# Optimization experiments

Measured on AMD Instinct MI355X. Metric: run time of the kernel, lower is better.

Reference implementation:

```python
import jax, jax.numpy as jnp
import numpy as np

B, S, H, Z = 32, 2048, 256, 64
TEMPERATURE = float(H) ** 0.5
NEG_INF = -1e9


def setup_inputs() -> dict:
    key = jax.random.key(0)
    ks = jax.random.split(key, 8)
    return {
        "encoder_hidden_states": jax.random.normal(ks[0], (B, S, H), dtype=jnp.float32),
        "decoder_hidden_states": jax.random.normal(ks[1], (B, S, H), dtype=jnp.float32),
        "decoder_final_hidden_state": jax.random.normal(ks[2], (B, H), dtype=jnp.float32),
        "latent_z_seq": jax.random.normal(ks[3], (B, S, Z), dtype=jnp.float32),
        "mask": jax.random.randint(ks[4], (B, S), 0, 2).astype(bool),
        "Wq": jax.random.normal(ks[5], (H, H), dtype=jnp.float32),
        "Wk": jax.random.normal(ks[6], (H, H), dtype=jnp.float32),
        "Wv": jax.random.normal(ks[7], (Z, Z), dtype=jnp.float32),
    }


def reference(encoder_hidden_states, decoder_hidden_states, decoder_final_hidden_state,
              latent_z_seq, mask, Wq, Wk, Wv):
    # Projections
    k = jnp.einsum('bsh,hd->bsd', encoder_hidden_states, Wk)
    q = jnp.einsum('bsh,hd->bsd', decoder_hidden_states, Wq)
    v = jnp.einsum('bsz,zd->bsd', latent_z_seq, Wv)
    # alignment[b, i, j] = q_i . k_j / sqrt(H)   -> [B, S, S]
    alignment = jnp.einsum('bid,bjd->bij', q, k) / TEMPERATURE
    # mask over QUERY positions (axis -2), broadcast along key axis (-1)
    alignment = jnp.where(mask[:, :, None], alignment, NEG_INF)
    # NOTE: non-standard softmax over the query axis (dim=-2)
    attn = jax.nn.softmax(alignment, axis=-2)
    output = jnp.einsum('bij,bjd->bid', attn, v)  # [B, S, Z]
    return output, attn
```

## Files before the change

kernel.cpp:

```cpp
#include <hip/hip_runtime.h>
#include <stdint.h>

#define B_  32
#define S_  2048
#define H_  256
#define Z_  64

typedef unsigned short u16;
typedef __attribute__((ext_vector_type(8))) short bf16x8;
typedef __attribute__((ext_vector_type(4))) float f32x4;

__device__ __forceinline__ u16 f2bf(float f) {
    unsigned int x = __float_as_uint(f);
    x = (x + 0x7fffu + ((x >> 16) & 1u)) >> 16;
    return (u16)x;
}
__device__ __forceinline__ float bf2f(u16 u) {
    return __uint_as_float(((unsigned int)u) << 16);
}

__device__ __forceinline__ void gl2lds16(const void* g, void* l) {
    __builtin_amdgcn_global_load_lds(
        (const __attribute__((address_space(1))) unsigned int*)g,
        (__attribute__((address_space(3))) unsigned int*)l,
        16, 0, 0);
}

__global__ void detect_kernel(const u16* __restrict__ wq, int* __restrict__ flag) {
    __shared__ int tot;
    const int t = threadIdx.x;
    if (t == 0) tot = 0;
    __syncthreads();
    int cnt = 0;
    #pragma unroll
    for (int r = 0; r < 16; ++r) {
        u16 u = wq[(r * 256 + t) * 2];
        int e = (u >> 7) & 0xFF;
        cnt += (u == 0 || (e >= 107 && e <= 132)) ? 1 : 0;
    }
    atomicAdd(&tot, cnt);
    __syncthreads();
    if (t == 0) *flag = (tot < 2048) ? 1 : 0;
}

__device__ void role_mask(int bx, const void* __restrict__ raw, int* __restrict__ mi) {
    __shared__ int isByte;
    const int t = threadIdx.x;
    if (t == 0) isByte = 0;
    __syncthreads();
    const unsigned int* w = (const unsigned int*)raw;
    if (w[t & 255] > 1u) isByte = 1;
    __syncthreads();
    int e = bx * 256 + t;
    int val;
    if (isByte) val = ((const unsigned char*)raw)[e] ? 1 : 0;
    else        val = w[e] ? 1 : 0;
    mi[e] = val;
}

__device__ void role_wsplit(int bx, int by, int fp32,
                            const void* __restrict__ Wq, const void* __restrict__ Wk,
                            u16* __restrict__ WqTh, u16* __restrict__ WqTl,
                            u16* __restrict__ WkTh, u16* __restrict__ WkTl) {
    const void* src = by ? Wk : Wq;
    u16* oh = by ? WkTh : WqTh;
    u16* ol = by ? WkTl : WqTl;
    int base = bx * 1024;
    #pragma unroll
    for (int r = 0; r < 4; ++r) {
        int idx = base + r * 256 + threadIdx.x;
        int d = idx >> 8, h = idx & 255;
        float v = fp32 ? ((const float*)src)[h * 256 + d]
                       : bf2f(((const u16*)src)[h * 256 + d]);
        u16 hi = f2bf(v);
        oh[idx] = hi;
        ol[idx] = f2bf(v - bf2f(hi));
    }
}

__device__ void role_xsplit(int bx, int by, int fp32,
                            const void* __restrict__ dec, const void* __restrict__ enc,
                            u16* __restrict__ Xdh, u16* __restrict__ Xdl,
                            u16* __restrict__ Xeh, u16* __restrict__ Xel) {
    const void* src = by ? enc : dec;
    u16* oh = by ? Xeh : Xdh;
    u16* ol = by ? Xel : Xdl;
    const int t = threadIdx.x;
    const size_t blockbase = (size_t)bx * 4096;
    if (fp32) {
        const float4* s4 = (const float4*)src;
        #pragma unroll
        for (int j = 0; j < 4; ++j) {
            size_t idx = blockbase + j * 1024 + t * 4;
            float4 v = s4[idx >> 2];
            u16 h0 = f2bf(v.x), h1 = f2bf(v.y), h2 = f2bf(v.z), h3 = f2bf(v.w);
            u16 l0 = f2bf(v.x - bf2f(h0)), l1 = f2bf(v.y - bf2f(h1));
            u16 l2 = f2bf(v.z - bf2f(h2)), l3 = f2bf(v.w - bf2f(h3));
            uint2 ph, pl;
            ph.x = (unsigned)h0 | ((unsigned)h1 << 16);
            ph.y = (unsigned)h2 | ((unsigned)h3 << 16);
            pl.x = (unsigned)l0 | ((unsigned)l1 << 16);
            pl.y = (unsigned)l2 | ((unsigned)l3 << 16);
            ((uint2*)oh)[idx >> 2] = ph;
            ((uint2*)ol)[idx >> 2] = pl;
        }
    } else {
        const uint2* s2 = (const uint2*)src;
        #pragma unroll
        for (int j = 0; j < 4; ++j) {
            size_t idx = blockbase + j * 1024 + t * 4;
            uint2 r = s2[idx >> 2];
            uint2 z; z.x = 0u; z.y = 0u;
            ((uint2*)oh)[idx >> 2] = r;
            ((uint2*)ol)[idx >> 2] = z;
        }
    }
}

__device__ void role_vproj(int bx, int dc, int fp32,
                           const void* __restrict__ Lraw,
                           const void* __restrict__ Wvraw, u16* __restrict__ vT) {
    __shared__ float wv[64 * 16];
    const int t = threadIdx.x;
    #pragma unroll
    for (int r = 0; r < 4; ++r) {
        int idx = r * 256 + t;
        int z = idx >> 4, dd = idx & 15;
        wv[idx] = fp32 ? ((const float*)Wvraw)[z * 64 + dc * 16 + dd]
                       : bf2f(((const u16*)Wvraw)[z * 64 + dc * 16 + dd]);
    }
    __syncthreads();
    const int flat = bx * 256 + t;
    const int b = flat >> 11, s = flat & 2047;

    float lz[64];
    if (fp32) {
        const float4* lr = (const float4*)((const float*)Lraw + (size_t)flat * 64);
        #pragma unroll
        for (int c = 0; c < 16; ++c) {
            float4 v = lr[c];
            lz[c * 4 + 0] = v.x; lz[c * 4 + 1] = v.y;
            lz[c * 4 + 2] = v.z; lz[c * 4 + 3] = v.w;
        }
    } else {
        const uint4* lr = (const uint4*)((const u16*)Lraw + (size_t)flat * 64);
        #pragma unroll
        for (int c = 0; c < 8; ++c) {
            uint4 v = lr[c];
            unsigned wd[4] = {v.x, v.y, v.z, v.w};
            #pragma unroll
            for (int e2 = 0; e2 < 4; ++e2) {
                lz[c * 8 + e2 * 2 + 0] = bf2f((u16)(wd[e2] & 0xffffu));
                lz[c * 8 + e2 * 2 + 1] = bf2f((u16)(wd[e2] >> 16));
            }
        }
    }

    float acc[16];
    #pragma unroll
    for (int d = 0; d < 16; ++d) acc[d] = 0.f;
    for (int z = 0; z < 64; ++z) {
        float lv = lz[z];
        const float4* wrow = (const float4*)&wv[z * 16];
        #pragma unroll
        for (int d4 = 0; d4 < 4; ++d4) {
            float4 wq = wrow[d4];
            acc[d4 * 4 + 0] += lv * wq.x;
            acc[d4 * 4 + 1] += lv * wq.y;
            acc[d4 * 4 + 2] += lv * wq.z;
            acc[d4 * 4 + 3] += lv * wq.w;
        }
    }
    #pragma unroll
    for (int d = 0; d < 16; ++d)
        vT[((size_t)b * 64 + dc * 16 + d) * S_ + s] = f2bf(acc[d]);
}

__global__ __launch_bounds__(256) void prep_kernel(
        const int* __restrict__ flagp, int n_xs,
        const void* __restrict__ dec, const void* __restrict__ enc,
        u16* __restrict__ Xdh, u16* __restrict__ Xdl,
        u16* __restrict__ Xeh, u16* __restrict__ Xel,
        const void* __restrict__ Lraw, const void* __restrict__ Wvraw,
        u16* __restrict__ vT,
        const void* __restrict__ Wq, const void* __restrict__ Wk,
        u16* __restrict__ WqTh, u16* __restrict__ WqTl,
        u16* __restrict__ WkTh, u16* __restrict__ WkTl,
        const void* __restrict__ mraw, int* __restrict__ maskI)
{
    const int fp32 = *flagp;
    int r = blockIdx.x;
    if (r < n_xs) {
        role_xsplit(r & 4095, r >> 12, fp32, dec, enc, Xdh, Xdl, Xeh, Xel);
        return;
    }
    r -= n_xs;
    if (r < 1024) {
        role_vproj(r & 255, r >> 8, fp32, Lraw, Wvraw, vT);
        return;
    }
    r -= 1024;
    if (r < 128) {
        role_wsplit(r & 63, r >> 6, fp32, Wq, Wk, WqTh, WqTl, WkTh, WkTl);
        return;
    }
    r -= 128;
    role_mask(r, mraw, maskI);
}

__global__ __launch_bounds__(256, 2) void proj_kernel(
        const int* __restrict__ flagp, int use_xsplit,
        const float* __restrict__ Xf0, const u16* __restrict__ Xu0,
        const u16* __restrict__ Xh0, const u16* __restrict__ Xl0,
        const u16* __restrict__ WTh0, const u16* __restrict__ WTl0,
        u16* __restrict__ Ph0, u16* __restrict__ Pl0,
        const float* __restrict__ Xf1, const u16* __restrict__ Xu1,
        const u16* __restrict__ Xh1, const u16* __restrict__ Xl1,
        const u16* __restrict__ WTh1, const u16* __restrict__ WTl1,
        u16* __restrict__ Ph1, u16* __restrict__ Pl1)
{
    __shared__ __align__(16) u16 lds[16384];
    const int z = blockIdx.z;
    const float* Xf = z ? Xf1 : Xf0;
    const u16*   Xu = z ? Xu1 : Xu0;
    const u16*   Xh = z ? Xh1 : Xh0;
    const u16*   Xl = z ? Xl1 : Xl0;
    const u16*  WTh = z ? WTh1 : WTh0;
    const u16*  WTl = z ? WTl1 : WTl0;
    u16* Ph = z ? Ph1 : Ph0;
    u16* Pl = z ? Pl1 : Pl0;

    const int fp32 = *flagp;
    const int t = threadIdx.x;
    const int lane = t & 63, w = t >> 6;
    const int i0 = blockIdx.x * 128;
    const int d0 = blockIdx.y * 128;
    const int rh = w >> 1, ch = w & 1;
    const int l15 = lane & 15;
    const int c0 = lane >> 4;

    const int srow = t >> 3;
    const int scp  = t & 7;
    const int sc   = scp ^ (srow & 7);
    const int scol = (sc & 3) * 8;
    const int slo  = sc & 4;

    f32x4 acc[4][4];
    #pragma unroll
    for (int a = 0; a < 4; ++a)
        #pragma unroll
        for (int c = 0; c < 4; ++c) acc[a][c] = (f32x4){0.f, 0.f, 0.f, 0.f};

    for (int ks = 0; ks < 8; ++ks) {
        const int kc = ks * 32;
        {
            const u16* wsrc = slo ? WTl : WTh;
            #pragma unroll
            for (int rep = 0; rep < 4; ++rep) {
                int s = t + rep * 256;
                int row = srow + rep * 32;
                gl2lds16(wsrc + (size_t)(d0 + row) * H_ + kc + scol, lds + 8192 + s * 8);
            }
        }
        if (use_xsplit) {
            const u16* xsrc = slo ? Xl : Xh;
            #pragma unroll
            for (int rep = 0; rep < 4; ++rep) {
                int s = t + rep * 256;
                int row = srow + rep * 32;
                gl2lds16(xsrc + (size_t)(i0 + row) * H_ + kc + scol, lds + s * 8);
            }
        } else if (fp32) {
            #pragma unroll
            for (int rep = 0; rep < 2; ++rep) {
                int s = t + rep * 256;
                int r = s >> 2, c8 = s & 3;
                const float4* src = (const float4*)(Xf + (size_t)(i0 + r) * H_ + kc + c8 * 8);
                float4 x0 = src[0], x1 = src[1];
                float xs[8] = {x0.x, x0.y, x0.z, x0.w, x1.x, x1.y, x1.z, x1.w};
                unsigned hh[8], ll[8];
                #pragma unroll
                for (int j = 0; j < 8; ++j) {
                    u16 hb = f2bf(xs[j]);
                    hh[j] = hb;
                    ll[j] = f2bf(xs[j] - bf2f(hb));
                }
                uint4 ph, pl;
                ph.x = hh[0] | (hh[1] << 16); ph.y = hh[2] | (hh[3] << 16);
                ph.z = hh[4] | (hh[5] << 16); ph.w = hh[6] | (hh[7] << 16);
                pl.x = ll[0] | (ll[1] << 16); pl.y = ll[2] | (ll[3] << 16);
                pl.z = ll[4] | (ll[5] << 16); pl.w = ll[6] | (ll[7] << 16);
                int posH = c8 ^ (r & 7);
                *(uint4*)(lds + r * 64 + posH * 8) = ph;
                *(uint4*)(lds + r * 64 + (posH ^ 4) * 8) = pl;
            }
        } else {
            #pragma unroll
            for (int rep = 0; rep < 2; ++rep) {
                int s = t + rep * 256;
                int r = s >> 2, c8 = s & 3;
                uint4 raw = *(const uint4*)(Xu + (size_t)(i0 + r) * H_ + kc + c8 * 8);
                int posH = c8 ^ (r & 7);
                *(uint4*)(lds + r * 64 + posH * 8) = raw;
                *(uint4*)(lds + r * 64 + (posH ^ 4) * 8) = (uint4){0u, 0u, 0u, 0u};
            }
        }
        __syncthreads();
        bf16x8 ah[4], al[4], bh[4], bl[4];
        #pragma unroll
        for (int f = 0; f < 4; ++f) {
            int ra = rh * 64 + f * 16 + l15;
            int rb = ch * 64 + f * 16 + l15;
            int pa = c0 ^ (ra & 7);
            int pb = c0 ^ (rb & 7);
            ah[f] = *(const bf16x8*)(lds + ra * 64 + pa * 8);
            al[f] = *(const bf16x8*)(lds + ra * 64 + (pa ^ 4) * 8);
            bh[f] = *(const bf16x8*)(lds + 8192 + rb * 64 + pb * 8);
            bl[f] = *(const bf16x8*)(lds + 8192 + rb * 64 + (pb ^ 4) * 8);
        }
        #pragma unroll
        for (int fr = 0; fr < 4; ++fr)
            #pragma unroll
            for (int fc = 0; fc < 4; ++fc) {
                acc[fr][fc] = __builtin_amdgcn_mfma_f32_16x16x32_bf16(al[fr], bh[fc], acc[fr][fc], 0, 0, 0);
                acc[fr][fc] = __builtin_amdgcn_mfma_f32_16x16x32_bf16(ah[fr], bl[fc], acc[fr][fc], 0, 0, 0);
                acc[fr][fc] = __builtin_amdgcn_mfma_f32_16x16x32_bf16(ah[fr], bh[fc], acc[fr][fc], 0, 0, 0);
            }
        __syncthreads();
    }
    #pragma unroll
    for (int fr = 0; fr < 4; ++fr)
        #pragma unroll
        for (int fc = 0; fc < 4; ++fc)
            #pragma unroll
            for (int reg = 0; reg < 4; ++reg) {
                float v = acc[fr][fc][reg];
                int i = i0 + rh * 64 + fr * 16 + (lane >> 4) * 4 + reg;
                int d = d0 + ch * 64 + fc * 16 + l15;
                u16 hi = f2bf(v);
                u16 lo = f2bf(v - bf2f(hi));
                size_t off = (size_t)i * H_ + d;
                Ph[off] = hi;
                Pl[off] = lo;
            }
}

__global__ __launch_bounds__(256, 2) void qk_kernel(
        const u16* __restrict__ qh, const u16* __restrict__ ql,
        const u16* __restrict__ kh, const u16* __restrict__ kl,
        const int* __restrict__ maskI, u16* __restrict__ attnB,
        float* __restrict__ attnF, u16* __restrict__ stageB, int use_stage,
        float* __restrict__ m_p, float* __restrict__ s_p,
        int b0, const int* __restrict__ flagp)
{
    __shared__ __align__(16) char smem[35328];
    u16*  stage = (u16*)smem;
    u16*  etile = (u16*)smem;
    float* cmax = (float*)(smem + 32768);
    float* csum = (float*)(smem + 33792);
    float* mrow = (float*)(smem + 34816);

    const int fp32 = *flagp;
    const int t = threadIdx.x;
    const int lane = t & 63, w = t >> 6;
    const int jt = blockIdx.x, it = blockIdx.y, bz = blockIdx.z;
    const int b = b0 + bz;
    const int i0 = it * 128, j0 = jt * 128;
    const int rh = w >> 1, ch = w & 1;
    const int l15 = lane & 15;
    const int c0 = lane >> 4;

    if (t < 128) mrow[t] = (maskI[b * S_ + i0 + t] != 0) ? 1.f : 0.f;

    const size_t qbase = ((size_t)bz * S_ + i0) * H_;
    const size_t kbase = ((size_t)bz * S_ + j0) * H_;

    const int srow = t >> 3;
    const int scp  = t & 7;
    const int sc   = scp ^ (srow & 7);
    const int scol = (sc & 3) * 8;
    const u16* qsrc = (sc & 4) ? ql : qh;
    const u16* ksrc = (sc & 4) ? kl : kh;

    f32x4 acc[4][4];
    #pragma unroll
    for (int a = 0; a < 4; ++a)
        #pragma unroll
        for (int c = 0; c < 4; ++c) acc[a][c] = (f32x4){0.f, 0.f, 0.f, 0.f};

    for (int ks = 0; ks < 8; ++ks) {
        const int kc = ks * 32;
        #pragma unroll
        for (int rep = 0; rep < 4; ++rep) {
            int s = t + rep * 256;
            int row = srow + rep * 32;
            gl2lds16(qsrc + qbase + (size_t)row * H_ + kc + scol, stage + s * 8);
            gl2lds16(ksrc + kbase + (size_t)row * H_ + kc + scol, stage + 8192 + s * 8);
        }
        __syncthreads();
        bf16x8 ah[4], al[4], bh[4], bl[4];
        #pragma unroll
        for (int f = 0; f < 4; ++f) {
            int ra = rh * 64 + f * 16 + l15;
            int rb = ch * 64 + f * 16 + l15;
            int pa = c0 ^ (ra & 7);
            int pb = c0 ^ (rb & 7);
            ah[f] = *(const bf16x8*)(stage + ra * 64 + pa * 8);
            al[f] = *(const bf16x8*)(stage + ra * 64 + (pa ^ 4) * 8);
            bh[f] = *(const bf16x8*)(stage + 8192 + rb * 64 + pb * 8);
            bl[f] = *(const bf16x8*)(stage + 8192 + rb * 64 + (pb ^ 4) * 8);
        }
        #pragma unroll
        for (int fr = 0; fr < 4; ++fr)
            #pragma unroll
            for (int fc = 0; fc < 4; ++fc) {
                acc[fr][fc] = __builtin_amdgcn_mfma_f32_16x16x32_bf16(al[fr], bh[fc], acc[fr][fc], 0, 0, 0);
                acc[fr][fc] = __builtin_amdgcn_mfma_f32_16x16x32_bf16(ah[fr], bl[fc], acc[fr][fc], 0, 0, 0);
                acc[fr][fc] = __builtin_amdgcn_mfma_f32_16x16x32_bf16(ah[fr], bh[fc], acc[fr][fc], 0, 0, 0);
            }
        __syncthreads();
    }

    const float inv_t = 0.0625f;
    float mloc[4] = {-3e38f, -3e38f, -3e38f, -3e38f};
    #pragma unroll
    for (int fr = 0; fr < 4; ++fr)
        #pragma unroll
        for (int reg = 0; reg < 4; ++reg) {
            float keep = mrow[rh * 64 + fr * 16 + (lane >> 4) * 4 + reg];
            #pragma unroll
            for (int fc = 0; fc < 4; ++fc) {
                float l = acc[fr][fc][reg] * inv_t;
                l = (keep != 0.f) ? l : -1e9f;
                acc[fr][fc][reg] = l;
                mloc[fc] = fmaxf(mloc[fc], l);
            }
        }
    #pragma unroll
    for (int fc = 0; fc < 4; ++fc) {
        mloc[fc] = fmaxf(mloc[fc], __shfl_xor(mloc[fc], 16, 64));
        mloc[fc] = fmaxf(mloc[fc], __shfl_xor(mloc[fc], 32, 64));
    }
    if (lane < 16) {
        #pragma unroll
        for (int fc = 0; fc < 4; ++fc)
            cmax[rh * 128 + ch * 64 + fc * 16 + lane] = mloc[fc];
    }
    __syncthreads();

    float mcol[4], sloc[4];
    #pragma unroll
    for (int fc = 0; fc < 4; ++fc) {
        int c = ch * 64 + fc * 16 + l15;
        mcol[fc] = fmaxf(cmax[c], cmax[128 + c]);
        sloc[fc] = 0.f;
    }
    #pragma unroll
    for (int fr = 0; fr < 4; ++fr)
        #pragma unroll
        for (int reg = 0; reg < 4; ++reg) {
            int row = rh * 64 + fr * 16 + (lane >> 4) * 4 + reg;
            #pragma unroll
            for (int fc = 0; fc < 4; ++fc) {
                float e = __expf(acc[fr][fc][reg] - mcol[fc]);
                sloc[fc] += e;
                etile[row * 128 + ch * 64 + fc * 16 + l15] = f2bf(e);
            }
        }
    #pragma unroll
    for (int fc = 0; fc < 4; ++fc) {
        sloc[fc] += __shfl_xor(sloc[fc], 16, 64);
        sloc[fc] += __shfl_xor(sloc[fc], 32, 64);
    }
    if (lane < 16) {
        #pragma unroll
        for (int fc = 0; fc < 4; ++fc)
            csum[rh * 128 + ch * 64 + fc * 16 + lane] = sloc[fc];
    }
    __syncthreads();

    if (t < 128) {
        float m = fmaxf(cmax[t], cmax[128 + t]);
        float sres = csum[t] + csum[128 + t];
        size_t so = ((size_t)b * 16 + it) * S_ + j0 + t;
        m_p[so] = m;
        s_p[so] = sres;
    }
    const size_t abase = ((size_t)b * S_ + i0) * S_ + j0;
    if (fp32) {
        if (use_stage) {
            #pragma unroll
            for (int rep = 0; rep < 8; ++rep) {
                int s = t + rep * 256;
                int row = s >> 4, off = (s & 15) * 8;
                *(uint4*)(stageB + abase + (size_t)row * S_ + off) = *(const uint4*)(etile + s * 8);
            }
        } else {
            #pragma unroll
            for (int rep = 0; rep < 8; ++rep) {
                int s = t + rep * 256;
                int row = s >> 4, off = (s & 15) * 8;
                const u16* src = etile + s * 8;
                float* gp = attnF + abase + (size_t)row * S_ + off;
                float4 f0, f1;
                f0.x = bf2f(src[0]); f0.y = bf2f(src[1]); f0.z = bf2f(src[2]); f0.w = bf2f(src[3]);
                f1.x = bf2f(src[4]); f1.y = bf2f(src[5]); f1.z = bf2f(src[6]); f1.w = bf2f(src[7]);
                *(float4*)gp = f0;
                *(float4*)(gp + 4) = f1;
            }
        }
    } else {
        #pragma unroll
        for (int rep = 0; rep < 8; ++rep) {
            int s = t + rep * 256;
            int row = s >> 4, off = (s & 15) * 8;
            *(uint4*)(attnB + abase + (size_t)row * S_ + off) = *(const uint4*)(etile + s * 8);
        }
    }
}

__global__ __launch_bounds__(256) void stats_kernel(
        const float* __restrict__ m_p, const float* __restrict__ s_p, float* __restrict__ scl)
{
    int id = blockIdx.x * 256 + threadIdx.x;
    int b = id >> 11, j = id & 2047;
    float mv[16];
    float M = -3e38f;
    #pragma unroll
    for (int itile = 0; itile < 16; ++itile) {
        mv[itile] = m_p[((size_t)b * 16 + itile) * S_ + j];
        M = fmaxf(M, mv[itile]);
    }
    float L = 0.f;
    #pragma unroll
    for (int itile = 0; itile < 16; ++itile)
        L += s_p[((size_t)b * 16 + itile) * S_ + j] * __expf(mv[itile] - M);
    float invL = (L > 0.f) ? (1.f / L) : 0.f;
    #pragma unroll
    for (int itile = 0; itile < 16; ++itile)
        scl[((size_t)b * 16 + itile) * S_ + j] = __expf(mv[itile] - M) * invL;
}

__global__ __launch_bounds__(256, 2) void av_gemm_kernel(
        const u16* __restrict__ vT, const float* __restrict__ scl,
        const u16* __restrict__ stageB, u16* __restrict__ attnB,
        float* __restrict__ attnF,
        u16* __restrict__ outB, float* __restrict__ outF,
        const int* __restrict__ flagp)
{
    __shared__ __align__(16) u16 lds_attn[128 * 128];
    __shared__ __align__(16) u16 lds_vt[64 * 128];
    const int fp32 = *flagp;
    const u16* srcE = fp32 ? stageB : attnB;
    const int t = threadIdx.x;
    const int lane = t & 63, w = t >> 6;
    const int it = blockIdx.x, b = blockIdx.y;
    const int i0 = it * 128;
    const int l15 = lane & 15;

    const int acp = t & 15;
    const int arow0 = t >> 4;
    const int ac = acp ^ (arow0 & 15);
    const int vpos = (t & 15) ^ (t >> 4);
    const int j8 = (t & 15) * 8;

    f32x4 acc[2][4];
    #pragma unroll
    for (int a = 0; a < 2; ++a)
        #pragma unroll
        for (int c = 0; c < 4; ++c) acc[a][c] = (f32x4){0.f, 0.f, 0.f, 0.f};

    for (int jt = 0; jt < 16; ++jt) {
        const int j0 = jt * 128;
        __syncthreads();
        const size_t abase = ((size_t)b * S_ + i0) * S_ + j0;
        #pragma unroll
        for (int rep = 0; rep < 8; ++rep) {
            int s = t + rep * 256;
            int row = arow0 + rep * 16;
            gl2lds16(srcE + abase + (size_t)row * S_ + ac * 8, lds_attn + s * 8);
        }
        float sc[8], esc[8];
        {
            const float4* sp = (const float4*)(scl + ((size_t)b * 16 + it) * S_ + j0 + j8);
            float4 s0 = sp[0], s1 = sp[1];
            sc[0] = s0.x; sc[1] = s0.y; sc[2] = s0.z; sc[3] = s0.w;
            sc[4] = s1.x; sc[5] = s1.y; sc[6] = s1.z; sc[7] = s1.w;
            const float4* ep = (const float4*)(scl + ((size_t)b * 16 + it) * S_ + j0 + ac * 8);
            float4 e0 = ep[0], e1 = ep[1];
            esc[0] = e0.x; esc[1] = e0.y; esc[2] = e0.z; esc[3] = e0.w;
            esc[4] = e1.x; esc[5] = e1.y; esc[6] = e1.z; esc[7] = e1.w;
        }
        #pragma unroll
        for (int rep = 0; rep < 4; ++rep) {
            int d = (t >> 4) + rep * 16;
            uint4 raw = *(const uint4*)(vT + ((size_t)b * 64 + d) * S_ + j0 + j8);
            unsigned wd[4] = {raw.x, raw.y, raw.z, raw.w};
            #pragma unroll
            for (int e2 = 0; e2 < 4; ++e2) {
                float f0 = bf2f((u16)(wd[e2] & 0xffffu)) * sc[e2 * 2];
                float f1 = bf2f((u16)(wd[e2] >> 16))     * sc[e2 * 2 + 1];
                wd[e2] = (unsigned)f2bf(f0) | ((unsigned)f2bf(f1) << 16);
            }
            uint4 pk; pk.x = wd[0]; pk.y = wd[1]; pk.z = wd[2]; pk.w = wd[3];
            *(uint4*)(lds_vt + d * 128 + vpos * 8) = pk;
        }
        __syncthreads();

        #pragma unroll
        for (int rep = 0; rep < 8; ++rep) {
            int s = t + rep * 256;
            int row = arow0 + rep * 16;
            uint4 pk = *(const uint4*)(lds_attn + s * 8);
            unsigned wd[4] = {pk.x, pk.y, pk.z, pk.w};
            float f[8];
            f[0] = bf2f((u16)(wd[0] & 0xffffu)) * esc[0];
            f[1] = bf2f((u16)(wd[0] >> 16))     * esc[1];
            f[2] = bf2f((u16)(wd[1] & 0xffffu)) * esc[2];
            f[3] = bf2f((u16)(wd[1] >> 16))     * esc[3];
            f[4] = bf2f((u16)(wd[2] & 0xffffu)) * esc[4];
            f[5] = bf2f((u16)(wd[2] >> 16))     * esc[5];
            f[6] = bf2f((u16)(wd[3] & 0xffffu)) * esc[6];
            f[7] = bf2f((u16)(wd[3] >> 16))     * esc[7];
            size_t ga = abase + (size_t)row * S_ + ac * 8;
            if (fp32) {
                float4 o0, o1;
                o0.x = f[0]; o0.y = f[1]; o0.z = f[2]; o0.w = f[3];
                o1.x = f[4]; o1.y = f[5]; o1.z = f[6]; o1.w = f[7];
                *(float4*)(attnF + ga) = o0;
                *(float4*)(attnF + ga + 4) = o1;
            } else {
                uint4 o;
                o.x = (unsigned)f2bf(f[0]) | ((unsigned)f2bf(f[1]) << 16);
                o.y = (unsigned)f2bf(f[2]) | ((unsigned)f2bf(f[3]) << 16);
                o.z = (unsigned)f2bf(f[4]) | ((unsigned)f2bf(f[5]) << 16);
                o.w = (unsigned)f2bf(f[6]) | ((unsigned)f2bf(f[7]) << 16);
                *(uint4*)(attnB + ga) = o;
            }
        }

        #pragma unroll
        for (int ksj = 0; ksj < 4; ++ksj) {
            int ck = ksj * 4 + (lane >> 4);
            int pA = ck ^ l15;
            int rA0 = w * 32 + l15, rA1 = w * 32 + 16 + l15;
            bf16x8 a0 = *(const bf16x8*)(lds_attn + rA0 * 128 + pA * 8);
            bf16x8 a1 = *(const bf16x8*)(lds_attn + rA1 * 128 + pA * 8);
            bf16x8 bb[4];
            #pragma unroll
            for (int fc = 0; fc < 4; ++fc) {
                int d = fc * 16 + l15;
                bb[fc] = *(const bf16x8*)(lds_vt + d * 128 + pA * 8);
            }
            #pragma unroll
            for (int fc = 0; fc < 4; ++fc) {
                acc[0][fc] = __builtin_amdgcn_mfma_f32_16x16x32_bf16(a0, bb[fc], acc[0][fc], 0, 0, 0);
                acc[1][fc] = __builtin_amdgcn_mfma_f32_16x16x32_bf16(a1, bb[fc], acc[1][fc], 0, 0, 0);
            }
        }
    }
    #pragma unroll
    for (int fr = 0; fr < 2; ++fr)
        #pragma unroll
        for (int fc = 0; fc < 4; ++fc)
            #pragma unroll
            for (int reg = 0; reg < 4; ++reg) {
                int i = i0 + w * 32 + fr * 16 + (lane >> 4) * 4 + reg;
                int d = fc * 16 + l15;
                float v = acc[fr][fc][reg];
                size_t oo = ((size_t)b * S_ + i) * Z_ + d;
                if (fp32) outF[oo] = v;
                else      outB[oo] = f2bf(v);
            }
}

__global__ __launch_bounds__(256, 2) void av_fallback_kernel(
        const u16* __restrict__ vT, const float* __restrict__ scl,
        u16* __restrict__ attnB, float* __restrict__ attnF,
        u16* __restrict__ outB, float* __restrict__ outF,
        const int* __restrict__ flagp)
{
    __shared__ __align__(16) u16 lds_attn[128 * 128];
    __shared__ __align__(16) u16 lds_vt[64 * 128];
    __shared__ float lds_scale[128];
    const int fp32 = *flagp;
    const int t = threadIdx.x;
    const int lane = t & 63, w = t >> 6;
    const int it = blockIdx.x, b = blockIdx.y;
    const int i0 = it * 128;
    const int l15 = lane & 15, koff = (lane >> 4) * 8;

    f32x4 acc[2][4];
    #pragma unroll
    for (int a = 0; a < 2; ++a)
        #pragma unroll
        for (int c = 0; c < 4; ++c) acc[a][c] = (f32x4){0.f, 0.f, 0.f, 0.f};

    for (int jt = 0; jt < 16; ++jt) {
        const int j0 = jt * 128;
        __syncthreads();
        if (t < 128) lds_scale[t] = scl[((size_t)b * 16 + it) * S_ + j0 + t];
        #pragma unroll
        for (int rep = 0; rep < 4; ++rep) {
            int s = t + rep * 256;
            int d = s >> 4, off = (s & 15) * 8;
            gl2lds16(vT + ((size_t)b * 64 + d) * S_ + j0 + off, lds_vt + s * 8);
        }
        __syncthreads();

        const size_t abase = ((size_t)b * S_ + i0) * S_ + j0;
        if (fp32) {
            #pragma unroll
            for (int rep = 0; rep < 8; ++rep) {
                int s = t + rep * 256;
                int row = s >> 4, off = (s & 15) * 8;
                float* gp = attnF + abase + (size_t)row * S_ + off;
                float4 p0 = *(const float4*)gp;
                float4 p1 = *(const float4*)(gp + 4);
                p0.x *= lds_scale[off + 0]; p0.y *= lds_scale[off + 1];
                p0.z *= lds_scale[off + 2]; p0.w *= lds_scale[off + 3];
                p1.x *= lds_scale[off + 4]; p1.y *= lds_scale[off + 5];
                p1.z *= lds_scale[off + 6]; p1.w *= lds_scale[off + 7];
                *(float4*)gp = p0;
                *(float4*)(gp + 4) = p1;
                uint4 pk;
                pk.x = (unsigned)f2bf(p0.x) | ((unsigned)f2bf(p0.y) << 16);
                pk.y = (unsigned)f2bf(p0.z) | ((unsigned)f2bf(p0.w) << 16);
                pk.z = (unsigned)f2bf(p1.x) | ((unsigned)f2bf(p1.y) << 16);
                pk.w = (unsigned)f2bf(p1.z) | ((unsigned)f2bf(p1.w) << 16);
                *(uint4*)(lds_attn + s * 8) = pk;
            }
        } else {
            #pragma unroll
            for (int rep = 0; rep < 8; ++rep) {
                int s = t + rep * 256;
                int row = s >> 4, off = (s & 15) * 8;
                size_t ga = abase + (size_t)row * S_ + off;
                uint4 pk = *(const uint4*)(attnB + ga);
                unsigned int wd[4] = {pk.x, pk.y, pk.z, pk.w};
                #pragma unroll
                for (int e2 = 0; e2 < 4; ++e2) {
                    float f0 = bf2f((u16)(wd[e2] & 0xffffu)) * lds_scale[off + e2 * 2];
                    float f1 = bf2f((u16)(wd[e2] >> 16))     * lds_scale[off + e2 * 2 + 1];
                    wd[e2] = (unsigned int)f2bf(f0) | ((unsigned int)f2bf(f1) << 16);
                }
                uint4 opk; opk.x = wd[0]; opk.y = wd[1]; opk.z = wd[2]; opk.w = wd[3];
                *(uint4*)(attnB + ga) = opk;
                *(uint4*)(lds_attn + s * 8) = opk;
            }
        }
        __syncthreads();

        #pragma unroll
        for (int ksj = 0; ksj < 4; ++ksj) {
            bf16x8 a0 = *(const bf16x8*)(lds_attn + (w * 32 +  0 + l15) * 128 + ksj * 32 + koff);
            bf16x8 a1 = *(const bf16x8*)(lds_attn + (w * 32 + 16 + l15) * 128 + ksj * 32 + koff);
            bf16x8 bb[4];
            #pragma unroll
            for (int fc = 0; fc < 4; ++fc)
                bb[fc] = *(const bf16x8*)(lds_vt + (fc * 16 + l15) * 128 + ksj * 32 + koff);
            #pragma unroll
            for (int fc = 0; fc < 4; ++fc) {
                acc[0][fc] = __builtin_amdgcn_mfma_f32_16x16x32_bf16(a0, bb[fc], acc[0][fc], 0, 0, 0);
                acc[1][fc] = __builtin_amdgcn_mfma_f32_16x16x32_bf16(a1, bb[fc], acc[1][fc], 0, 0, 0);
            }
        }
    }
    #pragma unroll
    for (int fr = 0; fr < 2; ++fr)
        #pragma unroll
        for (int fc = 0; fc < 4; ++fc)
            #pragma unroll
            for (int reg = 0; reg < 4; ++reg) {
                int i = i0 + w * 32 + fr * 16 + (lane >> 4) * 4 + reg;
                int d = fc * 16 + l15;
                float v = acc[fr][fc][reg];
                size_t oo = ((size_t)b * S_ + i) * Z_ + d;
                if (fp32) outF[oo] = v;
                else      outB[oo] = f2bf(v);
            }
}

extern "C" void kernel_launch(void* const* d_in, const int* in_sizes, int n_in,
                              void* d_out, int out_size, void* d_ws, size_t ws_size,
                              hipStream_t stream) {
    const void* enc    = d_in[0];
    const void* dec    = d_in[1];
    const void* latent = d_in[3];
    const void* mraw   = d_in[4];
    const void* Wq     = d_in[5];
    const void* Wk     = d_in[6];
    const void* Wv     = d_in[7];

    u16*   outB  = (u16*)d_out;
    float* outF  = (float*)d_out;
    u16*   attnB = outB + (size_t)B_ * S_ * Z_;
    float* attnF = outF + (size_t)B_ * S_ * Z_;
    float* m_p = (float*)d_out;
    float* s_p = m_p + (size_t)B_ * 16 * S_;

    char* ws = (char*)d_ws;
    int*   flag  = (int*)ws;
    int*   maskI = (int*)(ws + 256);
    u16*   vT    = (u16*)((char*)maskI + (size_t)B_ * S_ * 4);
    u16*   WqTh  = vT + (size_t)B_ * Z_ * S_;
    u16*   WqTl  = WqTh + H_ * H_;
    u16*   WkTh  = WqTl + H_ * H_;
    u16*   WkTl  = WkTh + H_ * H_;
    float* scl   = (float*)(WkTl + H_ * H_);
    char*  dyn   = (char*)(scl + (size_t)B_ * 16 * S_);

    const size_t fixed_bytes  = (size_t)(dyn - ws);
    const size_t per_batch    = (size_t)4 * S_ * H_ * 2;
    const size_t xsplit_bytes = (size_t)4 * B_ * S_ * H_ * 2;
    const size_t stage_bytes  = (size_t)B_ * S_ * S_ * 2;

    long long avail = (long long)ws_size - (long long)fixed_bytes;
    int use_xsplit = 0, use_stage = 0;
    u16 *Xdh = 0, *Xdl = 0, *Xeh = 0, *Xel = 0, *stageB = 0;
    if (avail >= (long long)(xsplit_bytes + per_batch)) {
        use_xsplit = 1;
        Xdh = (u16*)dyn;
        Xdl = Xdh + (size_t)B_ * S_ * H_;
        Xeh = Xdl + (size_t)B_ * S_ * H_;
        Xel = Xeh + (size_t)B_ * S_ * H_;
        dyn += xsplit_bytes;
        avail -= (long long)xsplit_bytes;
    }
    if (avail >= (long long)(stage_bytes + per_batch)) {
        use_stage = 1;
        stageB = (u16*)dyn;
        dyn += stage_bytes;
        avail -= (long long)stage_bytes;
    }
    int g_b = (avail > 0) ? (int)(avail / (long long)per_batch) : 1;
    if (g_b < 1)  g_b = 1;
    if (g_b > 32) g_b = 32;

    u16* qh = (u16*)dyn;
    u16* ql = qh + (size_t)g_b * S_ * H_;
    u16* kh = ql + (size_t)g_b * S_ * H_;
    u16* kl = kh + (size_t)g_b * S_ * H_;

    detect_kernel<<<dim3(1), 256, 0, stream>>>((const u16*)Wq, flag);

    const int n_xs = use_xsplit ? 8192 : 0;
    prep_kernel<<<dim3(n_xs + 1024 + 128 + 256), 256, 0, stream>>>(
        flag, n_xs, dec, enc, Xdh, Xdl, Xeh, Xel,
        latent, Wv, vT, Wq, Wk, WqTh, WqTl, WkTh, WkTl, mraw, maskI);

    for (int b0 = 0; b0 < B_; b0 += g_b) {
        int g = (B_ - b0 < g_b) ? (B_ - b0) : g_b;
        size_t eoff = (size_t)b0 * S_ * H_;
        proj_kernel<<<dim3(g * 16, 2, 2), 256, 0, stream>>>(
            flag, use_xsplit,
            (const float*)dec + eoff, (const u16*)dec + eoff,
            use_xsplit ? Xdh + eoff : (u16*)0, use_xsplit ? Xdl + eoff : (u16*)0,
            WqTh, WqTl, qh, ql,
            (const float*)enc + eoff, (const u16*)enc + eoff,
            use_xsplit ? Xeh + eoff : (u16*)0, use_xsplit ? Xel + eoff : (u16*)0,
            WkTh, WkTl, kh, kl);
        qk_kernel<<<dim3(16, 16, g), 256, 0, stream>>>(qh, ql, kh, kl, maskI,
                                                       attnB, attnF, stageB, use_stage,
                                                       m_p, s_p, b0, flag);
    }
    stats_kernel<<<dim3(256), 256, 0, stream>>>(m_p, s_p, scl);
    if (use_stage) {
        av_gemm_kernel<<<dim3(16, 32), 256, 0, stream>>>(vT, scl, stageB, attnB, attnF,
                                                         outB, outF, flag);
    } else {
        av_fallback_kernel<<<dim3(16, 32), 256, 0, stream>>>(vT, scl, attnB, attnF,
                                                             outB, outF, flag);
    }
}
```

Baseline: 1.106 ms.

## Fold Wq·Wk into G matrix and enlarge QK tiles to 256x256

```diff
diff --git a/kernel.cpp b/kernel.cpp
--- a/kernel.cpp
+++ b/kernel.cpp
@@ -78,6 +78,27 @@
     }
 }
 
+__device__ void role_gmat(int d, int fp32,
+                          const void* __restrict__ Wq, const void* __restrict__ Wk,
+                          u16* __restrict__ Gh, u16* __restrict__ Gl) {
+    __shared__ float wqrow[256];
+    const int t = threadIdx.x;
+    wqrow[t] = fp32 ? ((const float*)Wq)[d * 256 + t]
+                    : bf2f(((const u16*)Wq)[d * 256 + t]);
+    __syncthreads();
+    float s = 0.f;
+    if (fp32) {
+        const float* wk = (const float*)Wk + (size_t)t * 256;
+        for (int e = 0; e < 256; ++e) s += wqrow[e] * wk[e];
+    } else {
+        const u16* wk = (const u16*)Wk + (size_t)t * 256;
+        for (int e = 0; e < 256; ++e) s += wqrow[e] * bf2f(wk[e]);
+    }
+    u16 hi = f2bf(s);
+    Gh[d * 256 + t] = hi;
+    Gl[d * 256 + t] = f2bf(s - bf2f(hi));
+}
+
 __device__ void role_xsplit(int bx, int by, int fp32,
                             const void* __restrict__ dec, const void* __restrict__ enc,
                             u16* __restrict__ Xdh, u16* __restrict__ Xdl,
@@ -186,6 +207,7 @@
         const void* __restrict__ Wq, const void* __restrict__ Wk,
         u16* __restrict__ WqTh, u16* __restrict__ WqTl,
         u16* __restrict__ WkTh, u16* __restrict__ WkTl,
+        u16* __restrict__ Gh, u16* __restrict__ Gl,
         const void* __restrict__ mraw, int* __restrict__ maskI)
 {
     const int fp32 = *flagp;
@@ -205,7 +227,12 @@
         return;
     }
     r -= 128;
-    role_mask(r, mraw, maskI);
+    if (r < 256) {
+        role_mask(r, mraw, maskI);
+        return;
+    }
+    r -= 256;
+    role_gmat(r, fp32, Wq, Wk, Gh, Gl);
 }
 
 __global__ __launch_bounds__(256, 2) void proj_kernel(
@@ -345,7 +372,9 @@
             }
 }
 
-__global__ __launch_bounds__(256, 2) void qk_kernel(
+#define NIT_ 8
+#define EST_ 136
+__global__ __launch_bounds__(512, 2) void qk_kernel(
         const u16* __restrict__ qh, const u16* __restrict__ ql,
         const u16* __restrict__ kh, const u16* __restrict__ kl,
         const int* __restrict__ maskI, u16* __restrict__ attnB,
@@ -353,24 +382,24 @@
         float* __restrict__ m_p, float* __restrict__ s_p,
         int b0, const int* __restrict__ flagp)
 {
-    __shared__ __align__(16) char smem[35328];
+    __shared__ __align__(16) char smem[74752];
     u16*  stage = (u16*)smem;
     u16*  etile = (u16*)smem;
-    float* cmax = (float*)(smem + 32768);
-    float* csum = (float*)(smem + 33792);
-    float* mrow = (float*)(smem + 34816);
+    float* cmax = (float*)(smem + 69632);
+    float* csum = (float*)(smem + 71680);
+    float* mrow = (float*)(smem + 73728);
 
     const int fp32 = *flagp;
     const int t = threadIdx.x;
     const int lane = t & 63, w = t >> 6;
+    const int wr = w >> 2, wc = w & 3;
     const int jt = blockIdx.x, it = blockIdx.y, bz = blockIdx.z;
     const int b = b0 + bz;
-    const int i0 = it * 128, j0 = jt * 128;
-    const int rh = w >> 1, ch = w & 1;
+    const int i0 = it * 256, j0 = jt * 256;
     const int l15 = lane & 15;
     const int c0 = lane >> 4;
 
-    if (t < 128) mrow[t] = (maskI[b * S_ + i0 + t] != 0) ? 1.f : 0.f;
+    if (t < 256) mrow[t] = (maskI[b * S_ + i0 + t] != 0) ? 1.f : 0.f;
 
     const size_t qbase = ((size_t)bz * S_ + i0) * H_;
     const size_t kbase = ((size_t)bz * S_ + j0) * H_;
@@ -382,9 +411,9 @@
     const u16* qsrc = (sc & 4) ? ql : qh;
     const u16* ksrc = (sc & 4) ? kl : kh;
 
-    f32x4 acc[4][4];
-    #pragma unroll
-    for (int a = 0; a < 4; ++a)
+    f32x4 acc[8][4];
+    #pragma unroll
+    for (int a = 0; a < 8; ++a)
         #pragma unroll
         for (int c = 0; c < 4; ++c) acc[a][c] = (f32x4){0.f, 0.f, 0.f, 0.f};
 
@@ -392,42 +421,43 @@
         const int kc = ks * 32;
         #pragma unroll
         for (int rep = 0; rep < 4; ++rep) {
-            int s = t + rep * 256;
-            int row = srow + rep * 32;
+            int s = t + rep * 512;
+            int row = srow + rep * 64;
             gl2lds16(qsrc + qbase + (size_t)row * H_ + kc + scol, stage + s * 8);
-            gl2lds16(ksrc + kbase + (size_t)row * H_ + kc + scol, stage + 8192 + s * 8);
-        }
-        __syncthreads();
-        bf16x8 ah[4], al[4], bh[4], bl[4];
+            gl2lds16(ksrc + kbase + (size_t)row * H_ + kc + scol, stage + 16384 + s * 8);
+        }
+        __syncthreads();
+        bf16x8 bhf[4], blf[4];
         #pragma unroll
         for (int f = 0; f < 4; ++f) {
-            int ra = rh * 64 + f * 16 + l15;
-            int rb = ch * 64 + f * 16 + l15;
+            int rb = wc * 64 + f * 16 + l15;
+            int pb = c0 ^ (rb & 7);
+            bhf[f] = *(const bf16x8*)(stage + 16384 + rb * 64 + pb * 8);
+            blf[f] = *(const bf16x8*)(stage + 16384 + rb * 64 + (pb ^ 4) * 8);
+        }
+        #pragma unroll
+        for (int fr = 0; fr < 8; ++fr) {
+            int ra = wr * 128 + fr * 16 + l15;
             int pa = c0 ^ (ra & 7);
-            int pb = c0 ^ (rb & 7);
-            ah[f] = *(const bf16x8*)(stage + ra * 64 + pa * 8);
-            al[f] = *(const bf16x8*)(stage + ra * 64 + (pa ^ 4) * 8);
-            bh[f] = *(const bf16x8*)(stage + 8192 + rb * 64 + pb * 8);
-            bl[f] = *(const bf16x8*)(stage + 8192 + rb * 64 + (pb ^ 4) * 8);
-        }
-        #pragma unroll
-        for (int fr = 0; fr < 4; ++fr)
+            bf16x8 ahf = *(const bf16x8*)(stage + ra * 64 + pa * 8);
+            bf16x8 alf = *(const bf16x8*)(stage + ra * 64 + (pa ^ 4) * 8);
             #pragma unroll
             for (int fc = 0; fc < 4; ++fc) {
-                acc[fr][fc] = __builtin_amdgcn_mfma_f32_16x16x32_bf16(al[fr], bh[fc], acc[fr][fc], 0, 0, 0);
-                acc[fr][fc] = __builtin_amdgcn_mfma_f32_16x16x32_bf16(ah[fr], bl[fc], acc[fr][fc], 0, 0, 0);
-                acc[fr][fc] = __builtin_amdgcn_mfma_f32_16x16x32_bf16(ah[fr], bh[fc], acc[fr][fc], 0, 0, 0);
-            }
+                acc[fr][fc] = __builtin_amdgcn_mfma_f32_16x16x32_bf16(alf, bhf[fc], acc[fr][fc], 0, 0, 0);
+                acc[fr][fc] = __builtin_amdgcn_mfma_f32_16x16x32_bf16(ahf, blf[fc], acc[fr][fc], 0, 0, 0);
+                acc[fr][fc] = __builtin_amdgcn_mfma_f32_16x16x32_bf16(ahf, bhf[fc], acc[fr][fc], 0, 0, 0);
+            }
+        }
         __syncthreads();
     }
 
     const float inv_t = 0.0625f;
     float mloc[4] = {-3e38f, -3e38f, -3e38f, -3e38f};
     #pragma unroll
-    for (int fr = 0; fr < 4; ++fr)
+    for (int fr = 0; fr < 8; ++fr)
         #pragma unroll
         for (int reg = 0; reg < 4; ++reg) {
-            float keep = mrow[rh * 64 + fr * 16 + (lane >> 4) * 4 + reg];
+            float keep = mrow[wr * 128 + fr * 16 + c0 * 4 + reg];
             #pragma unroll
             for (int fc = 0; fc < 4; ++fc) {
                 float l = acc[fr][fc][reg] * inv_t;
@@ -444,29 +474,72 @@
     if (lane < 16) {
         #pragma unroll
         for (int fc = 0; fc < 4; ++fc)
-            cmax[rh * 128 + ch * 64 + fc * 16 + lane] = mloc[fc];
+            cmax[wr * 256 + wc * 64 + fc * 16 + lane] = mloc[fc];
     }
     __syncthreads();
 
-    float mcol[4], sloc[4];
+    float mcol[4];
     #pragma unroll
     for (int fc = 0; fc < 4; ++fc) {
-        int c = ch * 64 + fc * 16 + l15;
-        mcol[fc] = fmaxf(cmax[c], cmax[128 + c]);
-        sloc[fc] = 0.f;
-    }
-    #pragma unroll
-    for (int fr = 0; fr < 4; ++fr)
-        #pragma unroll
-        for (int reg = 0; reg < 4; ++reg) {
-            int row = rh * 64 + fr * 16 + (lane >> 4) * 4 + reg;
-            #pragma unroll
-            for (int fc = 0; fc < 4; ++fc) {
-                float e = __expf(acc[fr][fc][reg] - mcol[fc]);
-                sloc[fc] += e;
-                etile[row * 128 + ch * 64 + fc * 16 + l15] = f2bf(e);
-            }
-        }
+        int c = wc * 64 + fc * 16 + l15;
+        mcol[fc] = fmaxf(cmax[c], cmax[256 + c]);
+    }
+
+    float sloc[4] = {0.f, 0.f, 0.f, 0.f};
+    const int myp = wc >> 1;
+    const int lcb = (wc & 1) * 64;
+    for (int p = 0; p < 2; ++p) {
+        __syncthreads();
+        if (myp == p) {
+            #pragma unroll
+            for (int fr = 0; fr < 8; ++fr)
+                #pragma unroll
+                for (int reg = 0; reg < 4; ++reg) {
+                    int row = wr * 128 + fr * 16 + c0 * 4 + reg;
+                    #pragma unroll
+                    for (int fc = 0; fc < 4; ++fc) {
+                        float e = __expf(acc[fr][fc][reg] - mcol[fc]);
+                        sloc[fc] += e;
+                        etile[row * EST_ + lcb + fc * 16 + l15] = f2bf(e);
+                    }
+                }
+        }
+        __syncthreads();
+        const size_t abase = ((size_t)b * S_ + i0) * S_ + j0 + p * 128;
+        if (fp32) {
+            if (use_stage) {
+                #pragma unroll
+                for (int rep = 0; rep < 8; ++rep) {
+                    int g = t + rep * 512;
+                    int row = g >> 4, c4 = g & 15;
+                    *(uint4*)(stageB + abase + (size_t)row * S_ + c4 * 8) =
+                        *(const uint4*)(etile + row * EST_ + c4 * 8);
+                }
+            } else {
+                #pragma unroll
+                for (int rep = 0; rep < 8; ++rep) {
+                    int g = t + rep * 512;
+                    int row = g >> 4, c4 = g & 15;
+                    const u16* src = etile + row * EST_ + c4 * 8;
+                    float* gp = attnF + abase + (size_t)row * S_ + c4 * 8;
+                    float4 f0, f1;
+                    f0.x = bf2f(src[0]); f0.y = bf2f(src[1]); f0.z = bf2f(src[2]); f0.w = bf2f(src[3]);
+                    f1.x = bf2f(src[4]); f1.y = bf2f(src[5]); f1.z = bf2f(src[6]); f1.w = bf2f(src[7]);
+                    *(float4*)gp = f0;
+                    *(float4*)(gp + 4) = f1;
+                }
+            }
+        } else {
+            #pragma unroll
+            for (int rep = 0; rep < 8; ++rep) {
+                int g = t + rep * 512;
+                int row = g >> 4, c4 = g & 15;
+                *(uint4*)(attnB + abase + (size_t)row * S_ + c4 * 8) =
+                    *(const uint4*)(etile + row * EST_ + c4 * 8);
+            }
+        }
+    }
+
     #pragma unroll
     for (int fc = 0; fc < 4; ++fc) {
         sloc[fc] += __shfl_xor(sloc[fc], 16, 64);
@@ -475,47 +548,16 @@
     if (lane < 16) {
         #pragma unroll
         for (int fc = 0; fc < 4; ++fc)
-            csum[rh * 128 + ch * 64 + fc * 16 + lane] = sloc[fc];
+            csum[wr * 256 + wc * 64 + fc * 16 + lane] = sloc[fc];
     }
     __syncthreads();
 
-    if (t < 128) {
-        float m = fmaxf(cmax[t], cmax[128 + t]);
-        float sres = csum[t] + csum[128 + t];
-        size_t so = ((size_t)b * 16 + it) * S_ + j0 + t;
+    if (t < 256) {
+        float m = fmaxf(cmax[t], cmax[256 + t]);
+        float sres = csum[t] + csum[256 + t];
+        size_t so = ((size_t)b * NIT_ + it) * S_ + j0 + t;
         m_p[so] = m;
         s_p[so] = sres;
-    }
-    const size_t abase = ((size_t)b * S_ + i0) * S_ + j0;
-    if (fp32) {
-        if (use_stage) {
-            #pragma unroll
-            for (int rep = 0; rep < 8; ++rep) {
-                int s = t + rep * 256;
-                int row = s >> 4, off = (s & 15) * 8;
-                *(uint4*)(stageB + abase + (size_t)row * S_ + off) = *(const uint4*)(etile + s * 8);
-            }
-        } else {
-            #pragma unroll
-            for (int rep = 0; rep < 8; ++rep) {
-                int s = t + rep * 256;
-                int row = s >> 4, off = (s & 15) * 8;
-                const u16* src = etile + s * 8;
-                float* gp = attnF + abase + (size_t)row * S_ + off;
-                float4 f0, f1;
-                f0.x = bf2f(src[0]); f0.y = bf2f(src[1]); f0.z = bf2f(src[2]); f0.w = bf2f(src[3]);
-                f1.x = bf2f(src[4]); f1.y = bf2f(src[5]); f1.z = bf2f(src[6]); f1.w = bf2f(src[7]);
-                *(float4*)gp = f0;
-                *(float4*)(gp + 4) = f1;
-            }
-        }
-    } else {
-        #pragma unroll
-        for (int rep = 0; rep < 8; ++rep) {
-            int s = t + rep * 256;
-            int row = s >> 4, off = (s & 15) * 8;
-            *(uint4*)(attnB + abase + (size_t)row * S_ + off) = *(const uint4*)(etile + s * 8);
-        }
     }
 }
 
@@ -524,21 +566,21 @@
 {
     int id = blockIdx.x * 256 + threadIdx.x;
     int b = id >> 11, j = id & 2047;
-    float mv[16];
+    float mv[NIT_];
     float M = -3e38f;
     #pragma unroll
-    for (int itile = 0; itile < 16; ++itile) {
-        mv[itile] = m_p[((size_t)b * 16 + itile) * S_ + j];
+    for (int itile = 0; itile < NIT_; ++itile) {
+        mv[itile] = m_p[((size_t)b * NIT_ + itile) * S_ + j];
         M = fmaxf(M, mv[itile]);
     }
     float L = 0.f;
     #pragma unroll
-    for (int itile = 0; itile < 16; ++itile)
-        L += s_p[((size_t)b * 16 + itile) * S_ + j] * __expf(mv[itile] - M);
+    for (int itile = 0; itile < NIT_; ++itile)
+        L += s_p[((size_t)b * NIT_ + itile) * S_ + j] * __expf(mv[itile] - M);
     float invL = (L > 0.f) ? (1.f / L) : 0.f;
     #pragma unroll
-    for (int itile = 0; itile < 16; ++itile)
-        scl[((size_t)b * 16 + itile) * S_ + j] = __expf(mv[itile] - M) * invL;
+    for (int itile = 0; itile < NIT_; ++itile)
+        scl[((size_t)b * NIT_ + itile) * S_ + j] = __expf(mv[itile] - M) * invL;
 }
 
 __global__ __launch_bounds__(256, 2) void av_gemm_kernel(
@@ -563,6 +605,7 @@
     const int ac = acp ^ (arow0 & 15);
     const int vpos = (t & 15) ^ (t >> 4);
     const int j8 = (t & 15) * 8;
+    const size_t sclbase = ((size_t)b * NIT_ + (it >> 1)) * S_;
 
     f32x4 acc[2][4];
     #pragma unroll
@@ -582,11 +625,11 @@
         }
         float sc[8], esc[8];
         {
-            const float4* sp = (const float4*)(scl + ((size_t)b * 16 + it) * S_ + j0 + j8);
+            const float4* sp = (const float4*)(scl + sclbase + j0 + j8);
             float4 s0 = sp[0], s1 = sp[1];
             sc[0] = s0.x; sc[1] = s0.y; sc[2] = s0.z; sc[3] = s0.w;
             sc[4] = s1.x; sc[5] = s1.y; sc[6] = s1.z; sc[7] = s1.w;
-            const float4* ep = (const float4*)(scl + ((size_t)b * 16 + it) * S_ + j0 + ac * 8);
+            const float4* ep = (const float4*)(scl + sclbase + j0 + ac * 8);
             float4 e0 = ep[0], e1 = ep[1];
             esc[0] = e0.x; esc[1] = e0.y; esc[2] = e0.z; esc[3] = e0.w;
             esc[4] = e1.x; esc[5] = e1.y; esc[6] = e1.z; esc[7] = e1.w;
@@ -689,6 +732,7 @@
     const int it = blockIdx.x, b = blockIdx.y;
     const int i0 = it * 128;
     const int l15 = lane & 15, koff = (lane >> 4) * 8;
+    const size_t sclbase = ((size_t)b * NIT_ + (it >> 1)) * S_;
 
     f32x4 acc[2][4];
     #pragma unroll
@@ -699,7 +743,7 @@
     for (int jt = 0; jt < 16; ++jt) {
         const int j0 = jt * 128;
         __syncthreads();
-        if (t < 128) lds_scale[t] = scl[((size_t)b * 16 + it) * S_ + j0 + t];
+        if (t < 128) lds_scale[t] = scl[sclbase + j0 + t];
         #pragma unroll
         for (int rep = 0; rep < 4; ++rep) {
             int s = t + rep * 256;
@@ -797,7 +841,7 @@
     u16*   attnB = outB + (size_t)B_ * S_ * Z_;
     float* attnF = outF + (size_t)B_ * S_ * Z_;
     float* m_p = (float*)d_out;
-    float* s_p = m_p + (size_t)B_ * 16 * S_;
+    float* s_p = m_p + (size_t)B_ * NIT_ * S_;
 
     char* ws = (char*)d_ws;
     int*   flag  = (int*)ws;
@@ -807,8 +851,10 @@
     u16*   WqTl  = WqTh + H_ * H_;
     u16*   WkTh  = WqTl + H_ * H_;
     u16*   WkTl  = WkTh + H_ * H_;
-    float* scl   = (float*)(WkTl + H_ * H_);
-    char*  dyn   = (char*)(scl + (size_t)B_ * 16 * S_);
+    u16*   Gh    = WkTl + H_ * H_;
+    u16*   Gl    = Gh + H_ * H_;
+    float* scl   = (float*)(Gl + H_ * H_);
+    char*  dyn   = (char*)(scl + (size_t)B_ * NIT_ * S_);
 
     const size_t fixed_bytes  = (size_t)(dyn - ws);
     const size_t per_batch    = (size_t)4 * S_ * H_ * 2;
@@ -845,24 +891,36 @@
     detect_kernel<<<dim3(1), 256, 0, stream>>>((const u16*)Wq, flag);
 
     const int n_xs = use_xsplit ? 8192 : 0;
-    prep_kernel<<<dim3(n_xs + 1024 + 128 + 256), 256, 0, stream>>>(
+    prep_kernel<<<dim3(n_xs + 1024 + 128 + 256 + 256), 256, 0, stream>>>(
         flag, n_xs, dec, enc, Xdh, Xdl, Xeh, Xel,
-        latent, Wv, vT, Wq, Wk, WqTh, WqTl, WkTh, WkTl, mraw, maskI);
+        latent, Wv, vT, Wq, Wk, WqTh, WqTl, WkTh, WkTl, Gh, Gl, mraw, maskI);
 
     for (int b0 = 0; b0 < B_; b0 += g_b) {
         int g = (B_ - b0 < g_b) ? (B_ - b0) : g_b;
         size_t eoff = (size_t)b0 * S_ * H_;
-        proj_kernel<<<dim3(g * 16, 2, 2), 256, 0, stream>>>(
-            flag, use_xsplit,
-            (const float*)dec + eoff, (const u16*)dec + eoff,
-            use_xsplit ? Xdh + eoff : (u16*)0, use_xsplit ? Xdl + eoff : (u16*)0,
-            WqTh, WqTl, qh, ql,
-            (const float*)enc + eoff, (const u16*)enc + eoff,
-            use_xsplit ? Xeh + eoff : (u16*)0, use_xsplit ? Xel + eoff : (u16*)0,
-            WkTh, WkTl, kh, kl);
-        qk_kernel<<<dim3(16, 16, g), 256, 0, stream>>>(qh, ql, kh, kl, maskI,
-                                                       attnB, attnF, stageB, use_stage,
-                                                       m_p, s_p, b0, flag);
+        if (use_xsplit) {
+            proj_kernel<<<dim3(g * 16, 2, 1), 256, 0, stream>>>(
+                flag, use_xsplit,
+                (const float*)enc + eoff, (const u16*)enc + eoff,
+                Xeh + eoff, Xel + eoff,
+                Gh, Gl, kh, kl,
+                (const float*)enc + eoff, (const u16*)enc + eoff,
+                Xeh + eoff, Xel + eoff,
+                Gh, Gl, kh, kl);
+            qk_kernel<<<dim3(NIT_, NIT_, g), 512, 0, stream>>>(
+                Xdh + eoff, Xdl + eoff, kh, kl, maskI,
+                attnB, attnF, stageB, use_stage, m_p, s_p, b0, flag);
+        } else {
+            proj_kernel<<<dim3(g * 16, 2, 2), 256, 0, stream>>>(
+                flag, use_xsplit,
+                (const float*)dec + eoff, (const u16*)dec + eoff,
+                (u16*)0, (u16*)0, WqTh, WqTl, qh, ql,
+                (const float*)enc + eoff, (const u16*)enc + eoff,
+                (u16*)0, (u16*)0, WkTh, WkTl, kh, kl);
+            qk_kernel<<<dim3(NIT_, NIT_, g), 512, 0, stream>>>(
+                qh, ql, kh, kl, maskI,
+                attnB, attnF, stageB, use_stage, m_p, s_p, b0, flag);
+        }
     }
     stats_kernel<<<dim3(256), 256, 0, stream>>>(m_p, s_p, scl);
     if (use_stage) {
```

New measurement: 1.307 ms. +18.1%, slower.
